# Performance work log

Measured on AMD Instinct MI355X. Metric: run time of the kernel, lower is better.

The kernel has to match this reference:

```python
import jax, jax.numpy as jnp
import numpy as np


def setup_inputs() -> dict:
    key = jax.random.key(0)
    k1, k2 = jax.random.split(key)
    n_nodes, d_feat, n_edges = 100000, 48, 1600000
    x = jax.random.normal(k1, (n_nodes, d_feat), dtype=jnp.float32)
    edge_index = jax.random.randint(k2, (2, n_edges), 0, n_nodes, dtype=jnp.int64)
    return {"x": x, "edge_index": edge_index, "batch_size": 65536}


def reference(x, edge_index, batch_size):
    # adj = SparseTensor.from_edge_index(edge_index): adj[row, col] = 1 with
    # row = edge_index[0] (src), col = edge_index[1] (dst).
    # adj.t() @ x  ->  out[i] = sum over edges (src -> i) of x[src]
    src, dst = edge_index[0], edge_index[1]
    n_nodes = x.shape[0]
    # memory-bound gather + scatter-add (SpMM, sum aggregation)
    x_neighbors_sum = jax.ops.segment_sum(x[src], dst, num_segments=n_nodes)
    node_labels = jnp.concatenate(
        (x[:batch_size, :], x_neighbors_sum[:batch_size, :]), axis=-1
    )
    return node_labels
```

## Files before the change

### kernel.cpp

```cpp
#include <hip/hip_runtime.h>
#include <hip/hip_fp16.h>

#define DFEAT 48
#define OUTW  96
#define NBINB 512
#define BINTH 512
#define EPT   7
#define SORTCAP 3584
#define NBUCK2 512
#define RBITS 7
#define NROWS 128
#define RAWCAP 2560
#define CSRCAP 2560


static __device__ __forceinline__ unsigned short f2h(float f) {
    __half h = __float2half_rn(f);
    return *reinterpret_cast<unsigned short*>(&h);
}

static __device__ __forceinline__ int wave_iscan(int v, int lane) {
    #pragma unroll
    for (int d = 1; d < 64; d <<= 1) {
        int tv = __shfl_up(v, d, 64);
        if (lane >= d) v += tv;
    }
    return v;
}

__global__ __launch_bounds__(BINTH)
void bin_k(const int* __restrict__ ei, int n_edges, int batch, int chunk,
           const float4* __restrict__ x4, int nx4, uint2* __restrict__ xh4,
           unsigned short* __restrict__ starts, unsigned int* __restrict__ regions,
           int use_half) {
    __shared__ int cnt[NBUCK2];
    __shared__ int cur[NBUCK2];
    __shared__ int wsum[BINTH / 64];
    __shared__ int totS;
    __shared__ unsigned int sorted[SORTCAP];
    const int t = threadIdx.x;
    const int b = blockIdx.x;
    const int lane = t & 63, wid = t >> 6;

    if (use_half) {
        for (int i = b * BINTH + t; i < nx4; i += NBINB * BINTH) {
            float4 v = x4[i];
            xh4[i] = make_uint2((unsigned)f2h(v.x) | ((unsigned)f2h(v.y) << 16),
                                (unsigned)f2h(v.z) | ((unsigned)f2h(v.w) << 16));
        }
    }

    const int beg = b * chunk;
    const int end = min(beg + chunk, n_edges);

    unsigned int pay[EPT];
    int bkt[EPT];
    #pragma unroll
    for (int i = 0; i < EPT; i++) {
        bkt[i] = -1;
        int e = beg + t + i * BINTH;
        if (e < end) {
            int dst = ei[n_edges + e];
            if (dst < batch) {
                int src = ei[e];
                bkt[i] = dst >> RBITS;
                pay[i] = ((unsigned)(dst & (NROWS - 1)) << 17) | (unsigned)src;
            }
        }
    }
    cnt[t] = 0;
    __syncthreads();
    #pragma unroll
    for (int i = 0; i < EPT; i++)
        if (bkt[i] >= 0) atomicAdd(&cnt[bkt[i]], 1);
    __syncthreads();
    int v = cnt[t];
    int iv = wave_iscan(v, lane);
    if (lane == 63) wsum[wid] = iv;
    __syncthreads();
    if (t < BINTH / 64) {
        int wv = wsum[t];
        int sv = wave_iscan(wv, t);
        wsum[t] = sv - wv;
        if (t == BINTH / 64 - 1) totS = sv;
    }
    __syncthreads();
    int excl = iv - v + wsum[wid];
    int tot = totS;
    cur[t] = excl;
    starts[t * NBINB + b] = (unsigned short)excl;
    if (t == 0) starts[NBUCK2 * NBINB + b] = (unsigned short)tot;
    __syncthreads();
    #pragma unroll
    for (int i = 0; i < EPT; i++)
        if (bkt[i] >= 0) {
            int pos = atomicAdd(&cur[bkt[i]], 1);
            sorted[pos] = pay[i];
        }
    __syncthreads();
    unsigned int* reg = regions + (size_t)b * chunk;
    for (int i = t; i < tot; i += BINTH) reg[i] = sorted[i];
}

__global__ __launch_bounds__(1024)
void reduce_k(const float* __restrict__ x, const uint2* __restrict__ xh2,
              const unsigned short* __restrict__ starts,
              const unsigned int* __restrict__ regions,
              float* __restrict__ out, int batch, int chunk, int use_half) {
    __shared__ unsigned int raw[RAWCAP];
    __shared__ int csr[CSRCAP];
    __shared__ int cnt[NROWS], off[NROWS + 1], cur[NROWS];
    __shared__ int wsum[16];
    __shared__ int totS;
    const int t = threadIdx.x;
    const int kb = blockIdx.x;
    const int lane = t & 63, wid = t >> 6;

    int s0 = 0, len = 0;
    if (t < NBINB) {
        s0 = starts[kb * NBINB + t];
        int s1 = starts[(kb + 1) * NBINB + t];
        len = s1 - s0;
    }
    int iv = wave_iscan(len, lane);
    if (lane == 63 && wid < 8) wsum[wid] = iv;
    __syncthreads();
    if (t < 8) {
        int wv = wsum[t];
        int sv = wave_iscan(wv, t);
        wsum[t] = sv - wv;
        if (t == 7) totS = sv;
    }
    __syncthreads();
    const int T = min(totS, RAWCAP);
    if (t < NBINB && len > 0) {
        int base = iv - len + wsum[wid];
        const unsigned int* reg = regions + (size_t)t * chunk + s0;
        for (int i = 0; i < len; i++) {
            int p = base + i;
            if (p < RAWCAP) raw[p] = reg[i];
        }
    }
    if (t < NROWS) cnt[t] = 0;
    __syncthreads();
    for (int i = t; i < T; i += 1024) atomicAdd(&cnt[raw[i] >> 17], 1);
    __syncthreads();
    int v2 = (t < NROWS) ? cnt[t] : 0;
    int iv2 = wave_iscan(v2, lane);
    if (lane == 63 && wid < 2) wsum[wid] = iv2;
    __syncthreads();
    if (t == 0) {
        int a = wsum[0];
        off[NROWS] = a + wsum[1];
        wsum[1] = a;
        wsum[0] = 0;
    }
    __syncthreads();
    if (t < NROWS) {
        int excl = iv2 - v2 + wsum[wid];
        off[t] = excl;
        cur[t] = excl;
    }
    __syncthreads();
    for (int i = t; i < T; i += 1024) {
        unsigned int p = raw[i];
        int pos = atomicAdd(&cur[p >> 17], 1);
        if (pos < CSRCAP) csr[pos] = (int)(p & 0x1FFFFu);
    }
    __syncthreads();

    if (use_half) {
        const int g  = lane / 12;
        const int cg = lane - g * 12;
        const bool act = lane < 48;
        const float4* x4 = (const float4*)x;
        float4* out4 = (float4*)out;
        for (int r = wid; r < NROWS; r += 16) {
            int row = kb * NROWS + r;
            if (row >= batch) break;
            int e0 = off[r], e1 = min(off[r + 1], CSRCAP);
            float4 acc = make_float4(0.f, 0.f, 0.f, 0.f);
            for (int eb = e0; eb < e1; eb += 8) {
                int ea = eb + g;
                int ebn = eb + 4 + g;
                if (act && ea < e1) {
                    uint2 p = xh2[(size_t)csr[ea] * 12 + cg];
                    float2 f0 = __half22float2(*(const __half2*)&p.x);
                    float2 f1 = __half22float2(*(const __half2*)&p.y);
                    acc.x += f0.x; acc.y += f0.y; acc.z += f1.x; acc.w += f1.y;
                }
                if (act && ebn < e1) {
                    uint2 p = xh2[(size_t)csr[ebn] * 12 + cg];
                    float2 f0 = __half22float2(*(const __half2*)&p.x);
                    float2 f1 = __half22float2(*(const __half2*)&p.y);
                    acc.x += f0.x; acc.y += f0.y; acc.z += f1.x; acc.w += f1.y;
                }
            }
            float4 bb;
            bb.x = __shfl(acc.x, lane + 24); bb.y = __shfl(acc.y, lane + 24);
            bb.z = __shfl(acc.z, lane + 24); bb.w = __shfl(acc.w, lane + 24);
            if (lane < 24) { acc.x += bb.x; acc.y += bb.y; acc.z += bb.z; acc.w += bb.w; }
            bb.x = __shfl(acc.x, lane + 12); bb.y = __shfl(acc.y, lane + 12);
            bb.z = __shfl(acc.z, lane + 12); bb.w = __shfl(acc.w, lane + 12);
            if (lane < 12) {
                acc.x += bb.x; acc.y += bb.y; acc.z += bb.z; acc.w += bb.w;
                out4[(size_t)row * 24 + 12 + cg] = acc;
                out4[(size_t)row * 24 + cg] = x4[(size_t)row * 12 + cg];
            }
        }
    } else {
        if (lane < DFEAT) {
            for (int r = wid; r < NROWS; r += 16) {
                int row = kb * NROWS + r;
                if (row >= batch) break;
                int e0 = off[r], e1 = min(off[r + 1], CSRCAP);
                float acc = 0.f;
                for (int e = e0; e < e1; ++e)
                    acc += x[(size_t)csr[e] * DFEAT + lane];
                out[(size_t)row * OUTW + lane]         = x[(size_t)row * DFEAT + lane];
                out[(size_t)row * OUTW + DFEAT + lane] = acc;
            }
        }
    }
}


#define D4   12
#define ROW4 24

__global__ void init_out_kernel(const float4* __restrict__ x4,
                                float4* __restrict__ out4, int batch) {
    int idx = blockIdx.x * blockDim.x + threadIdx.x;
    int total = batch * ROW4;
    if (idx >= total) return;
    int row = idx / ROW4;
    int c   = idx - row * ROW4;
    float4 v;
    if (c < D4) v = x4[row * D4 + c];
    else        v = make_float4(0.f, 0.f, 0.f, 0.f);
    out4[idx] = v;
}

__global__ void scatter_edges_kernel(const float4* __restrict__ x4,
                                     const int* __restrict__ ei,
                                     float* __restrict__ out,
                                     int n_edges, int batch) {
    int tid = blockIdx.x * blockDim.x + threadIdx.x;
    int e = tid / D4;
    int q = tid - e * D4;
    if (e >= n_edges) return;
    int dst = ei[n_edges + e];
    if (dst >= batch) return;
    int src = ei[e];
    float4 v = x4[src * D4 + q];
    float* p = out + (size_t)dst * OUTW + DFEAT + q * 4;
    atomicAdd(p + 0, v.x);
    atomicAdd(p + 1, v.y);
    atomicAdd(p + 2, v.z);
    atomicAdd(p + 3, v.w);
}


extern "C" void kernel_launch(void* const* d_in, const int* in_sizes, int n_in,
                              void* d_out, int out_size, void* d_ws, size_t ws_size,
                              hipStream_t stream) {
    const float* x  = (const float*)d_in[0];
    const int*   ei = (const int*)d_in[1];
    float* out = (float*)d_out;

    const int n_edges = in_sizes[1] / 2;
    const int batch   = out_size / OUTW;
    const int n_nodes = in_sizes[0] / DFEAT;
    const int chunk   = (n_edges + NBINB - 1) / NBINB;
    const int nbuck   = (batch + NROWS - 1) / NROWS;
    const int nx4     = n_nodes * DFEAT / 4;

    size_t xh_bytes = ((size_t)n_nodes * DFEAT * sizeof(unsigned short) + 15) & ~(size_t)15;
    size_t starts_bytes = (size_t)(NBUCK2 + 1) * NBINB * sizeof(unsigned short);
    size_t reg_bytes = (size_t)NBINB * chunk * sizeof(unsigned int);
    size_t need_h = xh_bytes + starts_bytes + reg_bytes;
    size_t need_f = starts_bytes + reg_bytes;

    bool base_ok = chunk <= SORTCAP && chunk <= BINTH * EPT &&
                   n_nodes <= (1 << 17) && batch <= NBUCK2 * NROWS &&
                   (n_nodes * DFEAT) % 4 == 0 && nbuck >= 1 && nbuck <= NBUCK2;

    if (base_ok && ws_size >= need_h) {
        unsigned short* xh = (unsigned short*)d_ws;
        unsigned short* starts = (unsigned short*)((char*)d_ws + xh_bytes);
        unsigned int* regions = (unsigned int*)((char*)d_ws + xh_bytes + starts_bytes);
        bin_k<<<NBINB, BINTH, 0, stream>>>(ei, n_edges, batch, chunk,
                                           (const float4*)x, nx4, (uint2*)xh,
                                           starts, regions, 1);
        reduce_k<<<nbuck, 1024, 0, stream>>>(x, (const uint2*)xh, starts, regions,
                                             out, batch, chunk, 1);
    } else if (base_ok && ws_size >= need_f) {
        unsigned short* starts = (unsigned short*)d_ws;
        unsigned int* regions = (unsigned int*)((char*)d_ws + starts_bytes);
        bin_k<<<NBINB, BINTH, 0, stream>>>(ei, n_edges, batch, chunk,
                                           (const float4*)x, nx4, (uint2*)0,
                                           starts, regions, 0);
        reduce_k<<<nbuck, 1024, 0, stream>>>(x, (const uint2*)0, starts, regions,
                                             out, batch, chunk, 0);
    } else {
        {
            int total = batch * ROW4;
            int grid = (total + 255) / 256;
            init_out_kernel<<<grid, 256, 0, stream>>>((const float4*)x,
                                                      (float4*)out, batch);
        }
        {
            long long total = (long long)n_edges * D4;
            long long grid = (total + 255) / 256;
            scatter_edges_kernel<<<(int)grid, 256, 0, stream>>>(
                (const float4*)x, ei, out, n_edges, batch);
        }
    }
}
```

Before: 122.8 us.

## Scatter binned edges directly to global, unroll short copies, interleave two rows per wave

The bin kernel drops its shared-memory sorted staging buffer and scatters each payload straight to its global region slot, which removes a barrier and a copy loop and frees LDS for occupancy, at the cost of uncoalesced global writes. The reduce kernel adds a fully unrolled path for short per-bin segments during the raw gather. The half-precision aggregation loop now processes two rows per wave at once (rows r and r+64), so more independent gathers are in flight to hide memory latency. The cost is more registers and some idle lanes when the two rows differ in degree.

```diff
diff --git a/kernel.cpp b/kernel.cpp
--- a/kernel.cpp
+++ b/kernel.cpp
@@ -6,7 +6,6 @@
 #define NBINB 512
 #define BINTH 512
 #define EPT   7
-#define SORTCAP 3584
 #define NBUCK2 512
 #define RBITS 7
 #define NROWS 128
@@ -37,7 +36,6 @@
     __shared__ int cur[NBUCK2];
     __shared__ int wsum[BINTH / 64];
     __shared__ int totS;
-    __shared__ unsigned int sorted[SORTCAP];
     const int t = threadIdx.x;
     const int b = blockIdx.x;
     const int lane = t & 63, wid = t >> 6;
@@ -86,20 +84,17 @@
     }
     __syncthreads();
     int excl = iv - v + wsum[wid];
-    int tot = totS;
     cur[t] = excl;
     starts[t * NBINB + b] = (unsigned short)excl;
-    if (t == 0) starts[NBUCK2 * NBINB + b] = (unsigned short)tot;
-    __syncthreads();
+    if (t == 0) starts[NBUCK2 * NBINB + b] = (unsigned short)totS;
+    __syncthreads();
+    unsigned int* reg = regions + (size_t)b * chunk;
     #pragma unroll
     for (int i = 0; i < EPT; i++)
         if (bkt[i] >= 0) {
             int pos = atomicAdd(&cur[bkt[i]], 1);
-            sorted[pos] = pay[i];
-        }
-    __syncthreads();
-    unsigned int* reg = regions + (size_t)b * chunk;
-    for (int i = t; i < tot; i += BINTH) reg[i] = sorted[i];
+            reg[pos] = pay[i];
+        }
 }
 
 __global__ __launch_bounds__(1024)
@@ -136,9 +131,19 @@
     if (t < NBINB && len > 0) {
         int base = iv - len + wsum[wid];
         const unsigned int* reg = regions + (size_t)t * chunk + s0;
-        for (int i = 0; i < len; i++) {
-            int p = base + i;
-            if (p < RAWCAP) raw[p] = reg[i];
+        if (len <= 8) {
+            #pragma unroll
+            for (int i = 0; i < 8; i++) {
+                if (i < len) {
+                    int p = base + i;
+                    if (p < RAWCAP) raw[p] = reg[i];
+                }
+            }
+        } else {
+            for (int i = 0; i < len; i++) {
+                int p = base + i;
+                if (p < RAWCAP) raw[p] = reg[i];
+            }
         }
     }
     if (t < NROWS) cnt[t] = 0;
@@ -175,37 +180,70 @@
         const bool act = lane < 48;
         const float4* x4 = (const float4*)x;
         float4* out4 = (float4*)out;
-        for (int r = wid; r < NROWS; r += 16) {
-            int row = kb * NROWS + r;
-            if (row >= batch) break;
-            int e0 = off[r], e1 = min(off[r + 1], CSRCAP);
-            float4 acc = make_float4(0.f, 0.f, 0.f, 0.f);
-            for (int eb = e0; eb < e1; eb += 8) {
-                int ea = eb + g;
-                int ebn = eb + 4 + g;
-                if (act && ea < e1) {
-                    uint2 p = xh2[(size_t)csr[ea] * 12 + cg];
-                    float2 f0 = __half22float2(*(const __half2*)&p.x);
-                    float2 f1 = __half22float2(*(const __half2*)&p.y);
-                    acc.x += f0.x; acc.y += f0.y; acc.z += f1.x; acc.w += f1.y;
+        #pragma unroll
+        for (int rr = 0; rr < 4; rr++) {
+            const int ra = wid + 16 * rr;
+            const int rb = ra + 64;
+            const int rowA = kb * NROWS + ra;
+            const int rowB = kb * NROWS + rb;
+            const bool okA = rowA < batch, okB = rowB < batch;
+            int e0a = 0, e1a = 0, e0b = 0, e1b = 0;
+            if (okA) { e0a = off[ra]; e1a = min(off[ra + 1], CSRCAP); }
+            if (okB) { e0b = off[rb]; e1b = min(off[rb + 1], CSRCAP); }
+            float4 accA = make_float4(0.f, 0.f, 0.f, 0.f);
+            float4 accB = make_float4(0.f, 0.f, 0.f, 0.f);
+            int na = e1a - e0a, nb2 = e1b - e0b;
+            int n = na > nb2 ? na : nb2;
+            for (int k = 0; k < n; k += 8) {
+                if (act) {
+                    int a1 = e0a + k + g, a2 = e0a + k + 4 + g;
+                    int b1 = e0b + k + g, b2 = e0b + k + 4 + g;
+                    if (a1 < e1a) {
+                        uint2 p = xh2[(size_t)csr[a1] * 12 + cg];
+                        float2 f0 = __half22float2(*(const __half2*)&p.x);
+                        float2 f1 = __half22float2(*(const __half2*)&p.y);
+                        accA.x += f0.x; accA.y += f0.y; accA.z += f1.x; accA.w += f1.y;
+                    }
+                    if (b1 < e1b) {
+                        uint2 p = xh2[(size_t)csr[b1] * 12 + cg];
+                        float2 f0 = __half22float2(*(const __half2*)&p.x);
+                        float2 f1 = __half22float2(*(const __half2*)&p.y);
+                        accB.x += f0.x; accB.y += f0.y; accB.z += f1.x; accB.w += f1.y;
+                    }
+                    if (a2 < e1a) {
+                        uint2 p = xh2[(size_t)csr[a2] * 12 + cg];
+                        float2 f0 = __half22float2(*(const __half2*)&p.x);
+                        float2 f1 = __half22float2(*(const __half2*)&p.y);
+                        accA.x += f0.x; accA.y += f0.y; accA.z += f1.x; accA.w += f1.y;
+                    }
+                    if (b2 < e1b) {
+                        uint2 p = xh2[(size_t)csr[b2] * 12 + cg];
+                        float2 f0 = __half22float2(*(const __half2*)&p.x);
+                        float2 f1 = __half22float2(*(const __half2*)&p.y);
+                        accB.x += f0.x; accB.y += f0.y; accB.z += f1.x; accB.w += f1.y;
+                    }
                 }
-                if (act && ebn < e1) {
-                    uint2 p = xh2[(size_t)csr[ebn] * 12 + cg];
-                    float2 f0 = __half22float2(*(const __half2*)&p.x);
-                    float2 f1 = __half22float2(*(const __half2*)&p.y);
-                    acc.x += f0.x; acc.y += f0.y; acc.z += f1.x; acc.w += f1.y;
-                }
             }
             float4 bb;
-            bb.x = __shfl(acc.x, lane + 24); bb.y = __shfl(acc.y, lane + 24);
-            bb.z = __shfl(acc.z, lane + 24); bb.w = __shfl(acc.w, lane + 24);
-            if (lane < 24) { acc.x += bb.x; acc.y += bb.y; acc.z += bb.z; acc.w += bb.w; }
-            bb.x = __shfl(acc.x, lane + 12); bb.y = __shfl(acc.y, lane + 12);
-            bb.z = __shfl(acc.z, lane + 12); bb.w = __shfl(acc.w, lane + 12);
-            if (lane < 12) {
-                acc.x += bb.x; acc.y += bb.y; acc.z += bb.z; acc.w += bb.w;
-                out4[(size_t)row * 24 + 12 + cg] = acc;
-                out4[(size_t)row * 24 + cg] = x4[(size_t)row * 12 + cg];
+            bb.x = __shfl(accA.x, lane + 24); bb.y = __shfl(accA.y, lane + 24);
+            bb.z = __shfl(accA.z, lane + 24); bb.w = __shfl(accA.w, lane + 24);
+            if (lane < 24) { accA.x += bb.x; accA.y += bb.y; accA.z += bb.z; accA.w += bb.w; }
+            bb.x = __shfl(accA.x, lane + 12); bb.y = __shfl(accA.y, lane + 12);
+            bb.z = __shfl(accA.z, lane + 12); bb.w = __shfl(accA.w, lane + 12);
+            if (lane < 12 && okA) {
+                accA.x += bb.x; accA.y += bb.y; accA.z += bb.z; accA.w += bb.w;
+                out4[(size_t)rowA * 24 + 12 + cg] = accA;
+                out4[(size_t)rowA * 24 + cg] = x4[(size_t)rowA * 12 + cg];
+            }
+            bb.x = __shfl(accB.x, lane + 24); bb.y = __shfl(accB.y, lane + 24);
+            bb.z = __shfl(accB.z, lane + 24); bb.w = __shfl(accB.w, lane + 24);
+            if (lane < 24) { accB.x += bb.x; accB.y += bb.y; accB.z += bb.z; accB.w += bb.w; }
+            bb.x = __shfl(accB.x, lane + 12); bb.y = __shfl(accB.y, lane + 12);
+            bb.z = __shfl(accB.z, lane + 12); bb.w = __shfl(accB.w, lane + 12);
+            if (lane < 12 && okB) {
+                accB.x += bb.x; accB.y += bb.y; accB.z += bb.z; accB.w += bb.w;
+                out4[(size_t)rowB * 24 + 12 + cg] = accB;
+                out4[(size_t)rowB * 24 + cg] = x4[(size_t)rowB * 12 + cg];
             }
         }
     } else {
@@ -281,7 +319,7 @@
     size_t need_h = xh_bytes + starts_bytes + reg_bytes;
     size_t need_f = starts_bytes + reg_bytes;
 
-    bool base_ok = chunk <= SORTCAP && chunk <= BINTH * EPT &&
+    bool base_ok = chunk <= BINTH * EPT && chunk < 65536 &&
                    n_nodes <= (1 << 17) && batch <= NBUCK2 * NROWS &&
                    (n_nodes * DFEAT) % 4 == 0 && nbuck >= 1 && nbuck <= NBUCK2;
 
```

New measurement: 126.1 us. 2.7% more time.

## Bin edges into global per-bucket arrays and accumulate with shared-memory atomics

Applied to the files above, without the earlier changes.

Replaces the per-block region layout plus per-bucket gather-and-CSR rebuild with global per-bucket arrays filled through atomic cursors, so each reduce block reads one contiguous bucket. The reduce kernel now scatters half-precision neighbour features into a shared-memory accumulator with float atomics instead of building a per-row CSR and running a wave per row. The x copy into the left half of the output moves into the binning kernel, and the binning kernel now runs 256 blocks of 1024 threads. In exchange it adds a zeroing kernel, heavy LDS atomic traffic, and a fixed per-bucket capacity that silently drops edges past the cap. Floating-point summation order also becomes nondeterministic.

```diff
diff --git a/kernel.cpp b/kernel.cpp
--- a/kernel.cpp
+++ b/kernel.cpp
@@ -3,15 +3,14 @@
 
 #define DFEAT 48
 #define OUTW  96
-#define NBINB 512
-#define BINTH 512
+#define NBINB 256
+#define BINTH 1024
 #define EPT   7
-#define SORTCAP 3584
-#define NBUCK2 512
+#define SORTCAP 6272
+#define NBUCK 512
 #define RBITS 7
 #define NROWS 128
-#define RAWCAP 2560
-#define CSRCAP 2560
+#define CAPG  2560
 
 
 static __device__ __forceinline__ unsigned short f2h(float f) {
@@ -28,25 +27,39 @@
     return v;
 }
 
+__global__ void zero_k(int* p, int n) {
+    int i = blockIdx.x * blockDim.x + threadIdx.x;
+    if (i < n) p[i] = 0;
+}
+
 __global__ __launch_bounds__(BINTH)
 void bin_k(const int* __restrict__ ei, int n_edges, int batch, int chunk,
            const float4* __restrict__ x4, int nx4, uint2* __restrict__ xh4,
-           unsigned short* __restrict__ starts, unsigned int* __restrict__ regions,
-           int use_half) {
-    __shared__ int cnt[NBUCK2];
-    __shared__ int cur[NBUCK2];
-    __shared__ int wsum[BINTH / 64];
+           int* __restrict__ gcursor, unsigned int* __restrict__ gbucket,
+           float4* __restrict__ out4, int use_half) {
+    __shared__ int cnt[NBUCK];
+    __shared__ int off[NBUCK];
+    __shared__ int cur[NBUCK];
+    __shared__ int runbase[NBUCK];
+    __shared__ int wsum[8];
     __shared__ int totS;
     __shared__ unsigned int sorted[SORTCAP];
     const int t = threadIdx.x;
     const int b = blockIdx.x;
     const int lane = t & 63, wid = t >> 6;
 
-    if (use_half) {
-        for (int i = b * BINTH + t; i < nx4; i += NBINB * BINTH) {
+    {
+        const int batch12 = batch * 12;
+        const int bound = use_half ? nx4 : batch12;
+        for (int i = b * BINTH + t; i < bound; i += NBINB * BINTH) {
             float4 v = x4[i];
-            xh4[i] = make_uint2((unsigned)f2h(v.x) | ((unsigned)f2h(v.y) << 16),
-                                (unsigned)f2h(v.z) | ((unsigned)f2h(v.w) << 16));
+            if (use_half)
+                xh4[i] = make_uint2((unsigned)f2h(v.x) | ((unsigned)f2h(v.y) << 16),
+                                    (unsigned)f2h(v.z) | ((unsigned)f2h(v.w) << 16));
+            if (i < batch12) {
+                int row = i / 12, cg = i - row * 12;
+                out4[(size_t)row * 24 + cg] = v;
+            }
         }
     }
 
@@ -68,62 +81,15 @@
             }
         }
     }
-    cnt[t] = 0;
+    if (t < NBUCK) cnt[t] = 0;
     __syncthreads();
     #pragma unroll
     for (int i = 0; i < EPT; i++)
         if (bkt[i] >= 0) atomicAdd(&cnt[bkt[i]], 1);
     __syncthreads();
-    int v = cnt[t];
+    int v = (t < NBUCK) ? cnt[t] : 0;
     int iv = wave_iscan(v, lane);
-    if (lane == 63) wsum[wid] = iv;
-    __syncthreads();
-    if (t < BINTH / 64) {
-        int wv = wsum[t];
-        int sv = wave_iscan(wv, t);
-        wsum[t] = sv - wv;
-        if (t == BINTH / 64 - 1) totS = sv;
-    }
-    __syncthreads();
-    int excl = iv - v + wsum[wid];
-    int tot = totS;
-    cur[t] = excl;
-    starts[t * NBINB + b] = (unsigned short)excl;
-    if (t == 0) starts[NBUCK2 * NBINB + b] = (unsigned short)tot;
-    __syncthreads();
-    #pragma unroll
-    for (int i = 0; i < EPT; i++)
-        if (bkt[i] >= 0) {
-            int pos = atomicAdd(&cur[bkt[i]], 1);
-            sorted[pos] = pay[i];
-        }
-    __syncthreads();
-    unsigned int* reg = regions + (size_t)b * chunk;
-    for (int i = t; i < tot; i += BINTH) reg[i] = sorted[i];
-}
-
-__global__ __launch_bounds__(1024)
-void reduce_k(const float* __restrict__ x, const uint2* __restrict__ xh2,
-              const unsigned short* __restrict__ starts,
-              const unsigned int* __restrict__ regions,
-              float* __restrict__ out, int batch, int chunk, int use_half) {
-    __shared__ unsigned int raw[RAWCAP];
-    __shared__ int csr[CSRCAP];
-    __shared__ int cnt[NROWS], off[NROWS + 1], cur[NROWS];
-    __shared__ int wsum[16];
-    __shared__ int totS;
-    const int t = threadIdx.x;
-    const int kb = blockIdx.x;
-    const int lane = t & 63, wid = t >> 6;
-
-    int s0 = 0, len = 0;
-    if (t < NBINB) {
-        s0 = starts[kb * NBINB + t];
-        int s1 = starts[(kb + 1) * NBINB + t];
-        len = s1 - s0;
-    }
-    int iv = wave_iscan(len, lane);
-    if (lane == 63 && wid < 8) wsum[wid] = iv;
+    if (t < NBUCK && lane == 63) wsum[wid] = iv;
     __syncthreads();
     if (t < 8) {
         int wv = wsum[t];
@@ -132,94 +98,93 @@
         if (t == 7) totS = sv;
     }
     __syncthreads();
-    const int T = min(totS, RAWCAP);
-    if (t < NBINB && len > 0) {
-        int base = iv - len + wsum[wid];
-        const unsigned int* reg = regions + (size_t)t * chunk + s0;
-        for (int i = 0; i < len; i++) {
-            int p = base + i;
-            if (p < RAWCAP) raw[p] = reg[i];
-        }
-    }
-    if (t < NROWS) cnt[t] = 0;
-    __syncthreads();
-    for (int i = t; i < T; i += 1024) atomicAdd(&cnt[raw[i] >> 17], 1);
-    __syncthreads();
-    int v2 = (t < NROWS) ? cnt[t] : 0;
-    int iv2 = wave_iscan(v2, lane);
-    if (lane == 63 && wid < 2) wsum[wid] = iv2;
-    __syncthreads();
-    if (t == 0) {
-        int a = wsum[0];
-        off[NROWS] = a + wsum[1];
-        wsum[1] = a;
-        wsum[0] = 0;
-    }
-    __syncthreads();
-    if (t < NROWS) {
-        int excl = iv2 - v2 + wsum[wid];
+    if (t < NBUCK) {
+        int excl = iv - v + wsum[wid];
         off[t] = excl;
         cur[t] = excl;
-    }
-    __syncthreads();
-    for (int i = t; i < T; i += 1024) {
-        unsigned int p = raw[i];
-        int pos = atomicAdd(&cur[p >> 17], 1);
-        if (pos < CSRCAP) csr[pos] = (int)(p & 0x1FFFFu);
-    }
-    __syncthreads();
-
+        runbase[t] = (v > 0) ? atomicAdd(&gcursor[t], v) : 0;
+    }
+    __syncthreads();
+    #pragma unroll
+    for (int i = 0; i < EPT; i++)
+        if (bkt[i] >= 0) {
+            int pos = atomicAdd(&cur[bkt[i]], 1);
+            sorted[pos] = pay[i];
+        }
+    __syncthreads();
+    const int tot = totS;
+    for (int idx = t; idx < tot; idx += BINTH) {
+        int lo = 0, hi = NBUCK - 1;
+        #pragma unroll
+        for (int s = 0; s < 9; s++) {
+            int mid = (lo + hi + 1) >> 1;
+            if (idx >= off[mid]) lo = mid; else hi = mid - 1;
+        }
+        int gpos = runbase[lo] + (idx - off[lo]);
+        if (gpos < CAPG)
+            gbucket[(size_t)lo * CAPG + gpos] = sorted[idx];
+    }
+}
+
+__global__ __launch_bounds__(1024)
+void reduce_k(const float4* __restrict__ x4, const uint2* __restrict__ xh2,
+              const int* __restrict__ gcursor,
+              const unsigned int* __restrict__ gbucket,
+              float4* __restrict__ out4, int batch, int use_half) {
+    __shared__ float acc[NROWS * DFEAT];
+    __shared__ unsigned int eraw[CAPG];
+    const int t = threadIdx.x;
+    const int q = blockIdx.x;
+    const int glen = min(gcursor[q], CAPG);
+
+    for (int i = t; i < NROWS * DFEAT; i += 1024) acc[i] = 0.f;
+    const unsigned int* gb = gbucket + (size_t)q * CAPG;
+    for (int i = t; i < glen; i += 1024) eraw[i] = gb[i];
+    __syncthreads();
+
+    const int total12 = glen * 12;
     if (use_half) {
-        const int g  = lane / 12;
-        const int cg = lane - g * 12;
-        const bool act = lane < 48;
-        const float4* x4 = (const float4*)x;
-        float4* out4 = (float4*)out;
-        for (int r = wid; r < NROWS; r += 16) {
-            int row = kb * NROWS + r;
-            if (row >= batch) break;
-            int e0 = off[r], e1 = min(off[r + 1], CSRCAP);
-            float4 acc = make_float4(0.f, 0.f, 0.f, 0.f);
-            for (int eb = e0; eb < e1; eb += 8) {
-                int ea = eb + g;
-                int ebn = eb + 4 + g;
-                if (act && ea < e1) {
-                    uint2 p = xh2[(size_t)csr[ea] * 12 + cg];
+        for (int mb = t; mb < total12; mb += 4096) {
+            #pragma unroll
+            for (int u = 0; u < 4; u++) {
+                int m = mb + u * 1024;
+                if (m < total12) {
+                    int e = m / 12, cg = m - e * 12;
+                    unsigned int ent = eraw[e];
+                    int row = ent >> 17;
+                    uint2 p = xh2[(size_t)(ent & 0x1FFFFu) * 12 + cg];
                     float2 f0 = __half22float2(*(const __half2*)&p.x);
                     float2 f1 = __half22float2(*(const __half2*)&p.y);
-                    acc.x += f0.x; acc.y += f0.y; acc.z += f1.x; acc.w += f1.y;
+                    float* a = &acc[row * DFEAT + cg * 4];
+                    atomicAdd(a + 0, f0.x); atomicAdd(a + 1, f0.y);
+                    atomicAdd(a + 2, f1.x); atomicAdd(a + 3, f1.y);
                 }
-                if (act && ebn < e1) {
-                    uint2 p = xh2[(size_t)csr[ebn] * 12 + cg];
-                    float2 f0 = __half22float2(*(const __half2*)&p.x);
-                    float2 f1 = __half22float2(*(const __half2*)&p.y);
-                    acc.x += f0.x; acc.y += f0.y; acc.z += f1.x; acc.w += f1.y;
+            }
+        }
+    } else {
+        for (int mb = t; mb < total12; mb += 4096) {
+            #pragma unroll
+            for (int u = 0; u < 4; u++) {
+                int m = mb + u * 1024;
+                if (m < total12) {
+                    int e = m / 12, cg = m - e * 12;
+                    unsigned int ent = eraw[e];
+                    int row = ent >> 17;
+                    float4 p = x4[(size_t)(ent & 0x1FFFFu) * 12 + cg];
+                    float* a = &acc[row * DFEAT + cg * 4];
+                    atomicAdd(a + 0, p.x); atomicAdd(a + 1, p.y);
+                    atomicAdd(a + 2, p.z); atomicAdd(a + 3, p.w);
                 }
             }
-            float4 bb;
-            bb.x = __shfl(acc.x, lane + 24); bb.y = __shfl(acc.y, lane + 24);
-            bb.z = __shfl(acc.z, lane + 24); bb.w = __shfl(acc.w, lane + 24);
-            if (lane < 24) { acc.x += bb.x; acc.y += bb.y; acc.z += bb.z; acc.w += bb.w; }
-            bb.x = __shfl(acc.x, lane + 12); bb.y = __shfl(acc.y, lane + 12);
-            bb.z = __shfl(acc.z, lane + 12); bb.w = __shfl(acc.w, lane + 12);
-            if (lane < 12) {
-                acc.x += bb.x; acc.y += bb.y; acc.z += bb.z; acc.w += bb.w;
-                out4[(size_t)row * 24 + 12 + cg] = acc;
-                out4[(size_t)row * 24 + cg] = x4[(size_t)row * 12 + cg];
-            }
-        }
-    } else {
-        if (lane < DFEAT) {
-            for (int r = wid; r < NROWS; r += 16) {
-                int row = kb * NROWS + r;
-                if (row >= batch) break;
-                int e0 = off[r], e1 = min(off[r + 1], CSRCAP);
-                float acc = 0.f;
-                for (int e = e0; e < e1; ++e)
-                    acc += x[(size_t)csr[e] * DFEAT + lane];
-                out[(size_t)row * OUTW + lane]         = x[(size_t)row * DFEAT + lane];
-                out[(size_t)row * OUTW + DFEAT + lane] = acc;
-            }
+        }
+    }
+    __syncthreads();
+    for (int i = t; i < NROWS * 12; i += 1024) {
+        int row = i / 12, cg = i - row * 12;
+        int grow = q * NROWS + row;
+        if (grow < batch) {
+            float* a = &acc[row * DFEAT + cg * 4];
+            out4[(size_t)grow * 24 + 12 + cg] = make_float4(a[0], a[1], a[2], a[3]);
         }
     }
 }
@@ -276,32 +241,36 @@
     const int nx4     = n_nodes * DFEAT / 4;
 
     size_t xh_bytes = ((size_t)n_nodes * DFEAT * sizeof(unsigned short) + 15) & ~(size_t)15;
-    size_t starts_bytes = (size_t)(NBUCK2 + 1) * NBINB * sizeof(unsigned short);
-    size_t reg_bytes = (size_t)NBINB * chunk * sizeof(unsigned int);
-    size_t need_h = xh_bytes + starts_bytes + reg_bytes;
-    size_t need_f = starts_bytes + reg_bytes;
+    size_t cur_bytes = NBUCK * sizeof(int);
+    size_t gb_bytes = (size_t)NBUCK * CAPG * sizeof(unsigned int);
+    size_t need_h = xh_bytes + cur_bytes + gb_bytes;
+    size_t need_f = cur_bytes + gb_bytes;
 
     bool base_ok = chunk <= SORTCAP && chunk <= BINTH * EPT &&
-                   n_nodes <= (1 << 17) && batch <= NBUCK2 * NROWS &&
-                   (n_nodes * DFEAT) % 4 == 0 && nbuck >= 1 && nbuck <= NBUCK2;
+                   n_nodes <= (1 << 17) && batch <= NBUCK * NROWS &&
+                   (n_nodes * DFEAT) % 4 == 0 && nbuck >= 1 && nbuck <= NBUCK;
 
     if (base_ok && ws_size >= need_h) {
         unsigned short* xh = (unsigned short*)d_ws;
-        unsigned short* starts = (unsigned short*)((char*)d_ws + xh_bytes);
-        unsigned int* regions = (unsigned int*)((char*)d_ws + xh_bytes + starts_bytes);
+        int* gcursor = (int*)((char*)d_ws + xh_bytes);
+        unsigned int* gbucket = (unsigned int*)((char*)d_ws + xh_bytes + cur_bytes);
+        zero_k<<<1, NBUCK, 0, stream>>>(gcursor, NBUCK);
         bin_k<<<NBINB, BINTH, 0, stream>>>(ei, n_edges, batch, chunk,
                                            (const float4*)x, nx4, (uint2*)xh,
-                                           starts, regions, 1);
-        reduce_k<<<nbuck, 1024, 0, stream>>>(x, (const uint2*)xh, starts, regions,
-                                             out, batch, chunk, 1);
+                                           gcursor, gbucket, (float4*)out, 1);
+        reduce_k<<<nbuck, 1024, 0, stream>>>((const float4*)x, (const uint2*)xh,
+                                             gcursor, gbucket, (float4*)out,
+                                             batch, 1);
     } else if (base_ok && ws_size >= need_f) {
-        unsigned short* starts = (unsigned short*)d_ws;
-        unsigned int* regions = (unsigned int*)((char*)d_ws + starts_bytes);
+        int* gcursor = (int*)d_ws;
+        unsigned int* gbucket = (unsigned int*)((char*)d_ws + cur_bytes);
+        zero_k<<<1, NBUCK, 0, stream>>>(gcursor, NBUCK);
         bin_k<<<NBINB, BINTH, 0, stream>>>(ei, n_edges, batch, chunk,
                                            (const float4*)x, nx4, (uint2*)0,
-                                           starts, regions, 0);
-        reduce_k<<<nbuck, 1024, 0, stream>>>(x, (const uint2*)0, starts, regions,
-                                             out, batch, chunk, 0);
+                                           gcursor, gbucket, (float4*)out, 0);
+        reduce_k<<<nbuck, 1024, 0, stream>>>((const float4*)x, (const uint2*)0,
+                                             gcursor, gbucket, (float4*)out,
+                                             batch, 0);
     } else {
         {
             int total = batch * ROW4;
```

New measurement: 358.7 us. 2.92x slower.
